# Kernel tuning notes

Hardware: AMD Instinct MI355X
Metric: run time of the kernel (lower is better)

Reference implementation:

```python
import jax, jax.numpy as jnp
import numpy as np

EPS = 1e-5
C, FR, T = 256, 7, 251  # channel, frequency, time
B = 32


def _bn(x, p, axis):
    # p: stacked [gamma, beta, running_mean, running_var] (eval-mode BatchNorm)
    g, b, m, v = p
    scale = g * jax.lax.rsqrt(v + EPS)
    shape = [1] * x.ndim
    shape[axis] = -1
    return x * scale.reshape(shape) + (b - m * scale).reshape(shape)


def _branch(xr, qw, qbn, kw, kbn, lbn):
    # xr: [N, Cin, L]. conv1x1 (no bias) + BN1d over channel axis.
    q = _bn(jnp.einsum('oc,ncl->nol', qw, xr), qbn, 1)
    k = _bn(jnp.einsum('oc,ncl->nol', kw, xr), kbn, 1)
    # adaptive_avg_pool2d((1, L)) on [N,1,Cin,L]: mean over channel axis, identity on L
    qv = q.mean(axis=1)  # [N, L]
    kv = k.mean(axis=1)  # [N, L]
    logits = qv[:, :, None] * kv[:, None, :]  # outer product == matmul(q^T, k): [N, L, L]
    g, b, m, v = lbn[:, 0]  # BatchNorm2d(1), eval mode -> scalar affine
    scale = g * jax.lax.rsqrt(v + EPS)
    w = jax.nn.softmax(logits * scale + (b - m * scale), axis=-1)
    # einsum 'bhxy,ihh->bhxy' == v * sum_i diag(w_i); return the diagonal sum [L]
    return jnp.einsum('nii->i', w)


def setup_inputs() -> dict:
    key = jax.random.key(0)
    ks = jax.random.split(key, 20)

    def w(k, o, i):
        return jax.random.normal(k, (o, i), jnp.float32) * 0.05

    def bn(k, n):
        k1, k2, k3, k4 = jax.random.split(k, 4)
        gamma = 1.0 + 0.1 * jax.random.normal(k1, (n,), jnp.float32)
        beta = 0.1 * jax.random.normal(k2, (n,), jnp.float32)
        mean = 0.1 * jax.random.normal(k3, (n,), jnp.float32)
        var = jnp.abs(1.0 + 0.1 * jax.random.normal(k4, (n,), jnp.float32))
        return jnp.stack([gamma, beta, mean, var])

    return {
        'x': jax.random.normal(ks[0], (B, C, FR, T), jnp.float32),
        'qc_w': w(ks[1], T, T), 'qc_bn': bn(ks[2], T),
        'kc_w': w(ks[3], T, T), 'kc_bn': bn(ks[4], T),
        'lc_bn': bn(ks[5], 1),
        'qf_w': w(ks[6], C, C), 'qf_bn': bn(ks[7], C),
        'kf_w': w(ks[8], C, C), 'kf_bn': bn(ks[9], C),
        'lf_bn': bn(ks[10], 1),
        'qt_w': w(ks[11], C, C), 'qt_bn': bn(ks[12], C),
        'kt_w': w(ks[13], C, C), 'kt_bn': bn(ks[14], C),
        'lt_bn': bn(ks[15], 1),
        'v_w': w(ks[16], C, C),
        'v_b': 0.05 * jax.random.normal(ks[17], (C,), jnp.float32),
        'v_bn': bn(ks[18], C),
    }


def reference(x, qc_w, qc_bn, kc_w, kc_bn, lc_bn,
              qf_w, qf_bn, kf_w, kf_bn, lf_bn,
              qt_w, qt_bn, kt_w, kt_bn, lt_bn,
              v_w, v_b, v_bn):
    b = x.shape[0]
    # x: [B, C, FR, T]
    x_c = x.transpose(0, 2, 3, 1).reshape(b * FR, T, C)   # conv over T channels
    x_f = x.transpose(0, 2, 1, 3).reshape(b * FR, C, T)   # conv over C channels
    x_t = x.transpose(0, 3, 1, 2).reshape(b * T, C, FR)   # conv over C channels
    dc = _branch(x_c, qc_w, qc_bn, kc_w, kc_bn, lc_bn)    # [C] (attention over channel axis of v)
    df = _branch(x_f, qf_w, qf_bn, kf_w, kf_bn, lf_bn)    # [T]
    dt = _branch(x_t, qt_w, qt_bn, kt_w, kt_bn, lt_bn)    # [FR]
    v = _bn(jnp.einsum('oc,bcxy->boxy', v_w, x) + v_b[None, :, None, None], v_bn, 1)
    # v_c + v_f + v_t + x, where each v_* = v scaled by summed attention diagonal
    return v * (dc[None, :, None, None] + dt[None, None, :, None] + df[None, None, None, :]) + x
```

## Files before the change

kernel.cpp:

```cpp
#include <hip/hip_runtime.h>

typedef unsigned short u16;
typedef __attribute__((ext_vector_type(8))) short short8;
typedef __attribute__((ext_vector_type(4))) float float4v;
typedef __attribute__((ext_vector_type(4))) int int4v;
typedef __attribute__((ext_vector_type(2))) int int2v;

#define EPS 1e-5f
#define NC 256
#define NT 251
#define NF 7
#define NSP 1757
#define NB 32

#define OFF_QEC 0
#define OFF_KEC 256
#define OFF_QEF 512
#define OFF_KEF 768
#define OFF_QET 1024
#define OFF_KET 1280
#define OFF_VSC 1536
#define OFF_VOF 1792
#define OFF_CONST 2048
#define OFF_DC 2064
#define OFF_DF 2320
#define OFF_DT 2576
#define WS_END 2592
#define OFF_QT 2592
#define OFF_KT (OFF_QT+56320)
#define WS2_END (OFF_KT+56320)
#define OFF_WB16 WS2_END
#define WS3_END (WS2_END+32768)

__device__ __forceinline__ u16 f2b(float f) {
    unsigned int u = __float_as_uint(f);
    return (u16)((u + 0x7FFFu + ((u >> 16) & 1u)) >> 16);
}

__global__ __launch_bounds__(256) void prep_kernel(
    const float* qc_w, const float* qc_bn, const float* kc_w, const float* kc_bn, const float* lc_bn,
    const float* qf_w, const float* qf_bn, const float* kf_w, const float* kf_bn, const float* lf_bn,
    const float* qt_w, const float* qt_bn, const float* kt_w, const float* kt_bn, const float* lt_bn,
    const float* v_b, const float* v_bn, const float* v_w, float* ws)
{
    int tid = threadIdx.x;
    int blk = blockIdx.x;
    __shared__ float sc[256];
    __shared__ float red[256];
    if (blk < 24) {
        int m = blk >> 2, j = blk & 3;
        const float* w; const float* bn; float* out; int O;
        switch (m) {
            case 0: w=qc_w; bn=qc_bn; out=ws+OFF_QEC; O=NT; break;
            case 1: w=kc_w; bn=kc_bn; out=ws+OFF_KEC; O=NT; break;
            case 2: w=qf_w; bn=qf_bn; out=ws+OFF_QEF; O=NC; break;
            case 3: w=kf_w; bn=kf_bn; out=ws+OFF_KEF; O=NC; break;
            case 4: w=qt_w; bn=qt_bn; out=ws+OFF_QET; O=NC; break;
            default: w=kt_w; bn=kt_bn; out=ws+OFF_KET; O=NC; break;
        }
        if (tid < O) sc[tid] = bn[tid] * rsqrtf(bn[3*O+tid] + EPS);
        __syncthreads();
        int tl = tid & 63, kc4 = tid >> 6;
        int t = j*64 + tl;
        float acc = 0.f;
        if (t < O) {
            #pragma unroll 8
            for (int o = kc4; o < O; o += 4)
                acc = fmaf(sc[o], w[(size_t)o*O + t], acc);
        }
        red[tid] = acc;
        __syncthreads();
        if (tid < 64) {
            int tt = j*64 + tid;
            if (tt < O)
                out[tt] = (red[tid] + red[tid+64] + red[tid+128] + red[tid+192]) / (float)O;
        }
    } else if (blk == 24) {
        if (tid < NC) {
            float s = v_bn[tid] * rsqrtf(v_bn[3*NC+tid] + EPS);
            ws[OFF_VSC+tid] = s;
            ws[OFF_VOF+tid] = v_bn[NC+tid] - v_bn[2*NC+tid]*s + v_b[tid]*s;
        }
        if (tid == 0) {
            ws[OFF_CONST+6] = lc_bn[0] * rsqrtf(lc_bn[3] + EPS);
            ws[OFF_CONST+7] = lf_bn[0] * rsqrtf(lf_bn[3] + EPS);
            ws[OFF_CONST+8] = lt_bn[0] * rsqrtf(lt_bn[3] + EPS);
        }
        for (int i = tid; i < WS_END - OFF_DC; i += 256) ws[OFF_DC + i] = 0.f;
        const float* bns[6] = {qc_bn, kc_bn, qf_bn, kf_bn, qt_bn, kt_bn};
        #pragma unroll
        for (int m2 = 0; m2 < 6; ++m2) {
            int O = (m2 < 2) ? NT : NC;
            const float* bn = bns[m2];
            float bs = 0.f;
            if (tid < O) {
                float s = bn[tid] * rsqrtf(bn[3*O+tid] + EPS);
                bs = bn[O+tid] - bn[2*O+tid]*s;
            }
            red[tid] = bs; __syncthreads();
            for (int s2 = 128; s2 > 0; s2 >>= 1) { if (tid < s2) red[tid] += red[tid+s2]; __syncthreads(); }
            if (tid == 0) ws[OFF_CONST+m2] = red[0] / (float)O;
            __syncthreads();
        }
    } else {
        u16* wb = (u16*)(ws + OFF_WB16);
        int base = (blk - 25) * 8192;
        for (int i = tid; i < 8192; i += 256) {
            int idx = base + i;
            int r = idx >> 12, q = idx & 4095;
            int o = ((r >> 3) << 7) + ((q >> 9) << 4) + ((q >> 3) & 15);
            int k = ((r & 7) << 5) + (((q >> 7) & 3) << 3) + (q & 7);
            wb[idx] = f2b(v_w[o*NC + k]);
        }
    }
}

__global__ __launch_bounds__(512) void qkt_kernel(const float* __restrict__ x,
                                                  float* __restrict__ ws, int fuse_t)
{
    __shared__ float kvc[NC];
    __shared__ float kvf[NT];
    int tid = threadIdx.x;
    int n = blockIdx.x;
    int b = n / NF, f = n % NF;
    const float* xb = x + (size_t)b*NC*NSP + (size_t)f*NT;
    const float* cst = ws + OFF_CONST;

    float qc = 0.f, kc = 0.f, qf = 0.f, kf = 0.f;

    if (tid < 256) {
        const float* xrow = xb + (size_t)tid*NSP;
        const float* qeC = ws + OFF_QEC;  const float* keC = ws + OFF_KEC;
        #pragma unroll 16
        for (int t = 0; t < NT; ++t) {
            float xv = xrow[t];
            qc = fmaf(qeC[t], xv, qc);
            kc = fmaf(keC[t], xv, kc);
        }
        qc += cst[0]; kc += cst[1];
        kvc[tid] = kc;
    } else if (tid - 256 < NT) {
        int t = tid - 256;
        const float* xc = xb + t;
        const float* qeF = ws + OFF_QEF;  const float* keF = ws + OFF_KEF;
        const float* qeT = ws + OFF_QET;  const float* keT = ws + OFF_KET;
        float qt = 0.f, kt = 0.f;
        #pragma unroll 8
        for (int ch = 0; ch < NC; ++ch) {
            float xv = xc[(size_t)ch*NSP];
            qf = fmaf(qeF[ch], xv, qf);
            kf = fmaf(keF[ch], xv, kf);
            qt = fmaf(qeT[ch], xv, qt);
            kt = fmaf(keT[ch], xv, kt);
        }
        qf += cst[2]; kf += cst[3];
        qt += cst[4]; kt += cst[5];
        kvf[t] = kf;
        if (fuse_t) {
            ws[OFF_QT + ((size_t)b*NT + t)*NF + f] = qt;
            ws[OFF_KT + ((size_t)b*NT + t)*NF + f] = kt;
        }
    }
    __syncthreads();

    if (tid < 256) {
        float s = cst[6];
        float qi = s * qc;
        float m0=-1e30f, m1=-1e30f, m2=-1e30f, m3=-1e30f;
        #pragma unroll 2
        for (int jj = 0; jj < NC; jj += 4) {
            m0 = fmaxf(m0, qi*kvc[jj]);
            m1 = fmaxf(m1, qi*kvc[jj+1]);
            m2 = fmaxf(m2, qi*kvc[jj+2]);
            m3 = fmaxf(m3, qi*kvc[jj+3]);
        }
        float m = fmaxf(fmaxf(m0,m1), fmaxf(m2,m3));
        float d0=0.f, d1=0.f, d2=0.f, d3=0.f;
        #pragma unroll 2
        for (int jj = 0; jj < NC; jj += 4) {
            d0 += __expf(qi*kvc[jj]   - m);
            d1 += __expf(qi*kvc[jj+1] - m);
            d2 += __expf(qi*kvc[jj+2] - m);
            d3 += __expf(qi*kvc[jj+3] - m);
        }
        float den = (d0+d1)+(d2+d3);
        atomicAdd(&ws[OFF_DC + tid], __expf(qi*kc - m)/den);
    } else if (tid - 256 < NT) {
        int t = tid - 256;
        float s = cst[7];
        float qi = s * qf;
        float m0=-1e30f, m1=-1e30f, m2=-1e30f, m3=-1e30f;
        int jj = 0;
        #pragma unroll 2
        for (; jj + 3 < NT; jj += 4) {
            m0 = fmaxf(m0, qi*kvf[jj]);
            m1 = fmaxf(m1, qi*kvf[jj+1]);
            m2 = fmaxf(m2, qi*kvf[jj+2]);
            m3 = fmaxf(m3, qi*kvf[jj+3]);
        }
        for (; jj < NT; ++jj) m0 = fmaxf(m0, qi*kvf[jj]);
        float m = fmaxf(fmaxf(m0,m1), fmaxf(m2,m3));
        float d0=0.f, d1=0.f, d2=0.f, d3=0.f;
        jj = 0;
        #pragma unroll 2
        for (; jj + 3 < NT; jj += 4) {
            d0 += __expf(qi*kvf[jj]   - m);
            d1 += __expf(qi*kvf[jj+1] - m);
            d2 += __expf(qi*kvf[jj+2] - m);
            d3 += __expf(qi*kvf[jj+3] - m);
        }
        for (; jj < NT; ++jj) d0 += __expf(qi*kvf[jj] - m);
        float den = (d0+d1)+(d2+d3);
        atomicAdd(&ws[OFF_DF + t], __expf(qi*kf - m)/den);
    }
}

__global__ __launch_bounds__(256) void tsm_kernel(float* __restrict__ ws)
{
    __shared__ float dt_acc[NF];
    int tid = threadIdx.x, b = blockIdx.x;
    if (tid < NF) dt_acc[tid] = 0.f;
    __syncthreads();
    if (tid < NT) {
        float s = ws[OFF_CONST+8];
        const float* qp = ws + OFF_QT + ((size_t)b*NT + tid)*NF;
        const float* kp = ws + OFF_KT + ((size_t)b*NT + tid)*NF;
        float q[NF], k[NF];
        #pragma unroll
        for (int i = 0; i < NF; ++i) { q[i] = qp[i]; k[i] = kp[i]; }
        #pragma unroll
        for (int i = 0; i < NF; ++i) {
            float qi = s * q[i];
            float m = -1e30f;
            #pragma unroll
            for (int j = 0; j < NF; ++j) m = fmaxf(m, qi*k[j]);
            float den = 0.f;
            #pragma unroll
            for (int j = 0; j < NF; ++j) den += __expf(qi*k[j] - m);
            atomicAdd(&dt_acc[i], __expf(qi*k[i] - m)/den);
        }
    }
    __syncthreads();
    if (tid < NF) atomicAdd(&ws[OFF_DT + tid], dt_acc[tid]);
}

__global__ __launch_bounds__(256) void t_kernel(const float* __restrict__ x, float* __restrict__ ws)
{
    __shared__ float qs[32*NF], ks[32*NF], dt_acc[NF];
    int tid = threadIdx.x;
    int b  = blockIdx.x >> 3;
    int t0 = (blockIdx.x & 7) * 32;
    int tl = tid & 31, fr = tid >> 5;
    int t = t0 + tl;
    bool act = (fr < NF) && (t < NT);
    if (tid < NF) dt_acc[tid] = 0.f;

    float aq = 0.f, ak = 0.f;
    const float* qeT = ws + OFF_QET;
    const float* keT = ws + OFF_KET;
    if (act) {
        const float* xr = x + (size_t)b*NC*NSP + fr*NT + t;
        #pragma unroll 8
        for (int ch = 0; ch < NC; ++ch) {
            float xv = xr[(size_t)ch*NSP];
            aq = fmaf(qeT[ch], xv, aq);
            ak = fmaf(keT[ch], xv, ak);
        }
    }
    __syncthreads();
    if (act) {
        qs[tl*NF + fr] = aq + ws[OFF_CONST+4];
        ks[tl*NF + fr] = ak + ws[OFF_CONST+5];
    }
    __syncthreads();
    if (act) {
        float s = ws[OFF_CONST+8];
        float qi = s * qs[tl*NF + fr];
        float m = -1e30f;
        #pragma unroll
        for (int j = 0; j < NF; ++j) m = fmaxf(m, qi*ks[tl*NF + j]);
        float den = 0.f;
        #pragma unroll
        for (int j = 0; j < NF; ++j) den += __expf(qi*ks[tl*NF + j] - m);
        atomicAdd(&dt_acc[fr], __expf(qi*ks[tl*NF + fr] - m)/den);
    }
    __syncthreads();
    if (tid < NF) atomicAdd(&ws[OFF_DT + tid], dt_acc[tid]);
}

template<int WBF>
__global__ __launch_bounds__(256) void main_kernel(
    const float* __restrict__ x, const float* __restrict__ vw,
    const float* __restrict__ ws, float* __restrict__ out)
{
    __shared__ u16 Ws[8*512];
    __shared__ unsigned int Xs[8*256];
    __shared__ float vsL[128], voL[128], dcL[128], dtfL[128];

    int tid = threadIdx.x;
    int n0 = blockIdx.x * 128;
    int o0 = blockIdx.y * 128;
    int b  = blockIdx.z;
    const size_t xbase = (size_t)b * NC * NSP;

    if (tid < 128) {
        int o = o0 + tid;
        vsL[tid] = ws[OFF_VSC+o];
        voL[tid] = ws[OFF_VOF+o];
        dcL[tid] = ws[OFF_DC+o];
        int nn = n0 + tid; if (nn > NSP-1) nn = NSP-1;
        int ff = nn / NT, tt = nn - ff*NT;
        dtfL[tid] = ws[OFF_DT+ff] + ws[OFF_DF+tt];
    }

    int wv = tid >> 6, ln = tid & 63;
    int quad = ln >> 4, l16 = ln & 15;
    int wr = wv >> 1, wc = wv & 1;

    float4v acc[4][4] = {};

    int kgs = tid >> 5, nbs = tid & 31;
    int oo = tid >> 1, half = tid & 1;

    const u16* wbg = nullptr;
    if constexpr (WBF) wbg = (const u16*)(ws + OFF_WB16) + (size_t)blockIdx.y * 32768;

    for (int ks = 0; ks < 8; ++ks) {
        int k0 = ks * 32;
        if constexpr (WBF) {
            const int4v* wsrc = (const int4v*)(wbg + (size_t)ks*4096);
            *(int4v*)&Ws[tid*8]        = wsrc[tid];
            *(int4v*)&Ws[2048 + tid*8] = wsrc[256 + tid];
        } else {
            const float* wr4 = vw + (size_t)(o0+oo)*NC + k0 + half*16;
            union { u16 us[16]; short8 v[2]; } wb;
            #pragma unroll
            for (int c = 0; c < 16; ++c) wb.us[c] = f2b(wr4[c]);
            int frg = oo >> 4, o16 = oo & 15;
            #pragma unroll
            for (int qq = 0; qq < 2; ++qq) {
                int qd = 2*half + qq;
                *(short8*)&Ws[frg*512 + qd*128 + o16*8] = wb.v[qq];
            }
        }
        {
            int nbase = n0 + nbs*4;
            const float* xr = x + xbase + (size_t)(k0 + kgs*4)*NSP + nbase;
            float xv[4][4];
            if (nbase + 3 < NSP) {
                #pragma unroll
                for (int rr = 0; rr < 4; ++rr)
                    #pragma unroll
                    for (int i = 0; i < 4; ++i)
                        xv[rr][i] = xr[(size_t)rr*NSP + i];
            } else {
                #pragma unroll
                for (int rr = 0; rr < 4; ++rr)
                    #pragma unroll
                    for (int i = 0; i < 4; ++i)
                        xv[rr][i] = (nbase + i < NSP) ? xr[(size_t)rr*NSP + i] : 0.f;
            }
            unsigned int pk[8];
            #pragma unroll
            for (int i = 0; i < 4; ++i)
                #pragma unroll
                for (int jp = 0; jp < 2; ++jp)
                    pk[i*2+jp] = (unsigned int)f2b(xv[2*jp][i])
                               | ((unsigned int)f2b(xv[2*jp+1][i]) << 16);
            *(int4v*)&Xs[kgs*256 + nbs*8]     = *(int4v*)&pk[0];
            *(int4v*)&Xs[kgs*256 + nbs*8 + 4] = *(int4v*)&pk[4];
        }
        __syncthreads();

        short8 afr[4], bfr[4];
        #pragma unroll
        for (int fr = 0; fr < 4; ++fr)
            afr[fr] = *(short8*)&Ws[(wr*4+fr)*512 + ln*8];
        #pragma unroll
        for (int fc = 0; fc < 4; ++fc) {
            int nn = wc*64 + fc*16 + l16;
            int2v lo = *(int2v*)&Xs[(2*quad)*256 + nn*2];
            int2v hi = *(int2v*)&Xs[(2*quad+1)*256 + nn*2];
            union { int i4[4]; short8 v; } u;
            u.i4[0] = lo.x; u.i4[1] = lo.y; u.i4[2] = hi.x; u.i4[3] = hi.y;
            bfr[fc] = u.v;
        }
        #pragma unroll
        for (int fr = 0; fr < 4; ++fr)
            #pragma unroll
            for (int fc = 0; fc < 4; ++fc)
                acc[fr][fc] = __builtin_amdgcn_mfma_f32_16x16x32_bf16(
                    afr[fr], bfr[fc], acc[fr][fc], 0, 0, 0);
        __syncthreads();
    }

    #pragma unroll
    for (int fr = 0; fr < 4; ++fr) {
        #pragma unroll
        for (int r = 0; r < 4; ++r) {
            int ol = wr*64 + fr*16 + quad*4 + r;
            int o = o0 + ol;
            float vs = vsL[ol], vo = voL[ol], dcv = dcL[ol];
            const size_t orow = xbase + (size_t)o*NSP;
            #pragma unroll
            for (int fc = 0; fc < 4; ++fc) {
                int nl = wc*64 + fc*16 + l16;
                int nn = n0 + nl;
                if (nn < NSP) {
                    size_t gi = orow + nn;
                    out[gi] = (acc[fr][fc][r]*vs + vo)*(dcv + dtfL[nl]) + x[gi];
                }
            }
        }
    }
}

extern "C" void kernel_launch(void* const* d_in, const int* in_sizes, int n_in,
                              void* d_out, int out_size, void* d_ws, size_t ws_size,
                              hipStream_t stream)
{
    const float* x    = (const float*)d_in[0];
    const float* qc_w = (const float*)d_in[1];  const float* qc_bn = (const float*)d_in[2];
    const float* kc_w = (const float*)d_in[3];  const float* kc_bn = (const float*)d_in[4];
    const float* lc_bn= (const float*)d_in[5];
    const float* qf_w = (const float*)d_in[6];  const float* qf_bn = (const float*)d_in[7];
    const float* kf_w = (const float*)d_in[8];  const float* kf_bn = (const float*)d_in[9];
    const float* lf_bn= (const float*)d_in[10];
    const float* qt_w = (const float*)d_in[11]; const float* qt_bn = (const float*)d_in[12];
    const float* kt_w = (const float*)d_in[13]; const float* kt_bn = (const float*)d_in[14];
    const float* lt_bn= (const float*)d_in[15];
    const float* v_w  = (const float*)d_in[16]; const float* v_b   = (const float*)d_in[17];
    const float* v_bn = (const float*)d_in[18];
    float* ws = (float*)d_ws;
    float* out = (float*)d_out;

    int fuse_t = (ws_size >= (size_t)WS2_END * sizeof(float)) ? 1 : 0;
    int wbf    = (ws_size >= (size_t)WS3_END * sizeof(float)) ? 1 : 0;

    prep_kernel<<<wbf ? 33 : 25, 256, 0, stream>>>(qc_w,qc_bn,kc_w,kc_bn,lc_bn,
                                                   qf_w,qf_bn,kf_w,kf_bn,lf_bn,
                                                   qt_w,qt_bn,kt_w,kt_bn,lt_bn,
                                                   v_b,v_bn,v_w,ws);
    qkt_kernel<<<NB*NF, 512, 0, stream>>>(x, ws, fuse_t);
    if (fuse_t) tsm_kernel<<<NB, 256, 0, stream>>>(ws);
    else        t_kernel<<<NB*8, 256, 0, stream>>>(x, ws);
    if (wbf) main_kernel<1><<<dim3(14, 2, NB), 256, 0, stream>>>(x, v_w, ws, out);
    else     main_kernel<0><<<dim3(14, 2, NB), 256, 0, stream>>>(x, v_w, ws, out);
}
```

Baseline: 253.4 us.

## Double-buffer GEMM tiles, swizzle LDS, split qkt blocks, remap grid per XCD

The main GEMM kernel now double-buffers its weight and x tiles in LDS, issuing global loads for the next k-step before running the MFMAs on the current one. It also XOR-swizzles the Xs layout to cut bank conflicts and remaps the 1D grid so both o-halves of a tile land on the same XCD for L2 reuse. The qkt kernel is split into two blocks per (b,f), one per branch, each dividing its reduction across 512 threads, and the BN bias-mean reductions move from one serial block into the per-matrix prep blocks. The costs are more LDS, higher register pressure from holding prefetched data, and a remapping that assumes an 8-XCD round-robin dispatch.

```diff
diff --git a/kernel.cpp b/kernel.cpp
--- a/kernel.cpp
+++ b/kernel.cpp
@@ -32,6 +32,8 @@
 #define OFF_WB16 WS2_END
 #define WS3_END (WS2_END+32768)
 
+#define XSW(kg, w) ((kg)*256 + ((w) ^ ((((kg)>>1)&3)<<3)))
+
 __device__ __forceinline__ u16 f2b(float f) {
     unsigned int u = __float_as_uint(f);
     return (u16)((u + 0x7FFFu + ((u >> 16) & 1u)) >> 16);
@@ -75,6 +77,14 @@
             if (tt < O)
                 out[tt] = (red[tid] + red[tid+64] + red[tid+128] + red[tid+192]) / (float)O;
         }
+        if (j == 0) {
+            float bs = 0.f;
+            if (tid < O) bs = bn[O+tid] - bn[2*O+tid]*sc[tid];
+            __syncthreads();
+            red[tid] = bs; __syncthreads();
+            for (int s2 = 128; s2 > 0; s2 >>= 1) { if (tid < s2) red[tid] += red[tid+s2]; __syncthreads(); }
+            if (tid == 0) ws[OFF_CONST+m] = red[0] / (float)O;
+        }
     } else if (blk == 24) {
         if (tid < NC) {
             float s = v_bn[tid] * rsqrtf(v_bn[3*NC+tid] + EPS);
@@ -87,21 +97,6 @@
             ws[OFF_CONST+8] = lt_bn[0] * rsqrtf(lt_bn[3] + EPS);
         }
         for (int i = tid; i < WS_END - OFF_DC; i += 256) ws[OFF_DC + i] = 0.f;
-        const float* bns[6] = {qc_bn, kc_bn, qf_bn, kf_bn, qt_bn, kt_bn};
-        #pragma unroll
-        for (int m2 = 0; m2 < 6; ++m2) {
-            int O = (m2 < 2) ? NT : NC;
-            const float* bn = bns[m2];
-            float bs = 0.f;
-            if (tid < O) {
-                float s = bn[tid] * rsqrtf(bn[3*O+tid] + EPS);
-                bs = bn[O+tid] - bn[2*O+tid]*s;
-            }
-            red[tid] = bs; __syncthreads();
-            for (int s2 = 128; s2 > 0; s2 >>= 1) { if (tid < s2) red[tid] += red[tid+s2]; __syncthreads(); }
-            if (tid == 0) ws[OFF_CONST+m2] = red[0] / (float)O;
-            __syncthreads();
-        }
     } else {
         u16* wb = (u16*)(ws + OFF_WB16);
         int base = (blk - 25) * 8192;
@@ -118,100 +113,115 @@
 __global__ __launch_bounds__(512) void qkt_kernel(const float* __restrict__ x,
                                                   float* __restrict__ ws, int fuse_t)
 {
-    __shared__ float kvc[NC];
-    __shared__ float kvf[NT];
+    __shared__ float kv[NC];
+    __shared__ float p0[512], p1[512], p2[512], p3[512];
     int tid = threadIdx.x;
-    int n = blockIdx.x;
+    int bid = blockIdx.x;
+    int n = bid >> 1, role = bid & 1;
     int b = n / NF, f = n % NF;
     const float* xb = x + (size_t)b*NC*NSP + (size_t)f*NT;
     const float* cst = ws + OFF_CONST;
-
-    float qc = 0.f, kc = 0.f, qf = 0.f, kf = 0.f;
-
-    if (tid < 256) {
-        const float* xrow = xb + (size_t)tid*NSP;
+    int half = tid >> 8, lid = tid & 255;
+
+    if (role == 0) {
+        const float* xrow = xb + (size_t)lid*NSP;
         const float* qeC = ws + OFF_QEC;  const float* keC = ws + OFF_KEC;
+        float qc = 0.f, kc = 0.f;
+        int t0 = half ? 126 : 0, t1 = half ? NT : 126;
         #pragma unroll 16
-        for (int t = 0; t < NT; ++t) {
+        for (int t = t0; t < t1; ++t) {
             float xv = xrow[t];
             qc = fmaf(qeC[t], xv, qc);
             kc = fmaf(keC[t], xv, kc);
         }
-        qc += cst[0]; kc += cst[1];
-        kvc[tid] = kc;
-    } else if (tid - 256 < NT) {
-        int t = tid - 256;
-        const float* xc = xb + t;
-        const float* qeF = ws + OFF_QEF;  const float* keF = ws + OFF_KEF;
-        const float* qeT = ws + OFF_QET;  const float* keT = ws + OFF_KET;
-        float qt = 0.f, kt = 0.f;
-        #pragma unroll 8
-        for (int ch = 0; ch < NC; ++ch) {
-            float xv = xc[(size_t)ch*NSP];
-            qf = fmaf(qeF[ch], xv, qf);
-            kf = fmaf(keF[ch], xv, kf);
-            qt = fmaf(qeT[ch], xv, qt);
-            kt = fmaf(keT[ch], xv, kt);
-        }
-        qf += cst[2]; kf += cst[3];
-        qt += cst[4]; kt += cst[5];
-        kvf[t] = kf;
-        if (fuse_t) {
-            ws[OFF_QT + ((size_t)b*NT + t)*NF + f] = qt;
-            ws[OFF_KT + ((size_t)b*NT + t)*NF + f] = kt;
-        }
-    }
-    __syncthreads();
-
-    if (tid < 256) {
-        float s = cst[6];
-        float qi = s * qc;
-        float m0=-1e30f, m1=-1e30f, m2=-1e30f, m3=-1e30f;
-        #pragma unroll 2
-        for (int jj = 0; jj < NC; jj += 4) {
-            m0 = fmaxf(m0, qi*kvc[jj]);
-            m1 = fmaxf(m1, qi*kvc[jj+1]);
-            m2 = fmaxf(m2, qi*kvc[jj+2]);
-            m3 = fmaxf(m3, qi*kvc[jj+3]);
-        }
-        float m = fmaxf(fmaxf(m0,m1), fmaxf(m2,m3));
-        float d0=0.f, d1=0.f, d2=0.f, d3=0.f;
-        #pragma unroll 2
-        for (int jj = 0; jj < NC; jj += 4) {
-            d0 += __expf(qi*kvc[jj]   - m);
-            d1 += __expf(qi*kvc[jj+1] - m);
-            d2 += __expf(qi*kvc[jj+2] - m);
-            d3 += __expf(qi*kvc[jj+3] - m);
-        }
-        float den = (d0+d1)+(d2+d3);
-        atomicAdd(&ws[OFF_DC + tid], __expf(qi*kc - m)/den);
-    } else if (tid - 256 < NT) {
-        int t = tid - 256;
-        float s = cst[7];
-        float qi = s * qf;
-        float m0=-1e30f, m1=-1e30f, m2=-1e30f, m3=-1e30f;
-        int jj = 0;
-        #pragma unroll 2
-        for (; jj + 3 < NT; jj += 4) {
-            m0 = fmaxf(m0, qi*kvf[jj]);
-            m1 = fmaxf(m1, qi*kvf[jj+1]);
-            m2 = fmaxf(m2, qi*kvf[jj+2]);
-            m3 = fmaxf(m3, qi*kvf[jj+3]);
-        }
-        for (; jj < NT; ++jj) m0 = fmaxf(m0, qi*kvf[jj]);
-        float m = fmaxf(fmaxf(m0,m1), fmaxf(m2,m3));
-        float d0=0.f, d1=0.f, d2=0.f, d3=0.f;
-        jj = 0;
-        #pragma unroll 2
-        for (; jj + 3 < NT; jj += 4) {
-            d0 += __expf(qi*kvf[jj]   - m);
-            d1 += __expf(qi*kvf[jj+1] - m);
-            d2 += __expf(qi*kvf[jj+2] - m);
-            d3 += __expf(qi*kvf[jj+3] - m);
-        }
-        for (; jj < NT; ++jj) d0 += __expf(qi*kvf[jj] - m);
-        float den = (d0+d1)+(d2+d3);
-        atomicAdd(&ws[OFF_DF + t], __expf(qi*kf - m)/den);
+        p0[tid] = qc; p1[tid] = kc;
+        __syncthreads();
+        if (tid < 256) {
+            qc = p0[tid] + p0[tid+256] + cst[0];
+            kc = p1[tid] + p1[tid+256] + cst[1];
+            kv[tid] = kc;
+        }
+        __syncthreads();
+        if (tid < 256) {
+            float s = cst[6];
+            float qi = s * qc;
+            float m0=-1e30f, m1=-1e30f, m2=-1e30f, m3=-1e30f;
+            #pragma unroll 2
+            for (int jj = 0; jj < NC; jj += 4) {
+                m0 = fmaxf(m0, qi*kv[jj]);
+                m1 = fmaxf(m1, qi*kv[jj+1]);
+                m2 = fmaxf(m2, qi*kv[jj+2]);
+                m3 = fmaxf(m3, qi*kv[jj+3]);
+            }
+            float m = fmaxf(fmaxf(m0,m1), fmaxf(m2,m3));
+            float d0=0.f, d1=0.f, d2=0.f, d3=0.f;
+            #pragma unroll 2
+            for (int jj = 0; jj < NC; jj += 4) {
+                d0 += __expf(qi*kv[jj]   - m);
+                d1 += __expf(qi*kv[jj+1] - m);
+                d2 += __expf(qi*kv[jj+2] - m);
+                d3 += __expf(qi*kv[jj+3] - m);
+            }
+            float den = (d0+d1)+(d2+d3);
+            atomicAdd(&ws[OFF_DC + tid], __expf(qi*kv[tid] - m)/den);
+        }
+    } else {
+        float qf=0.f, kf=0.f, qt=0.f, kt=0.f;
+        if (lid < NT) {
+            const float* xc = xb + lid + (size_t)(half*128)*NSP;
+            const float* qeF = ws + OFF_QEF + half*128;  const float* keF = ws + OFF_KEF + half*128;
+            const float* qeT = ws + OFF_QET + half*128;  const float* keT = ws + OFF_KET + half*128;
+            #pragma unroll 8
+            for (int ch = 0; ch < 128; ++ch) {
+                float xv = xc[(size_t)ch*NSP];
+                qf = fmaf(qeF[ch], xv, qf);
+                kf = fmaf(keF[ch], xv, kf);
+                qt = fmaf(qeT[ch], xv, qt);
+                kt = fmaf(keT[ch], xv, kt);
+            }
+        }
+        p0[tid]=qf; p1[tid]=kf; p2[tid]=qt; p3[tid]=kt;
+        __syncthreads();
+        float qfv=0.f, kfv=0.f;
+        if (tid < NT) {
+            qfv = p0[tid] + p0[tid+256] + cst[2];
+            kfv = p1[tid] + p1[tid+256] + cst[3];
+            float qtv = p2[tid] + p2[tid+256] + cst[4];
+            float ktv = p3[tid] + p3[tid+256] + cst[5];
+            kv[tid] = kfv;
+            if (fuse_t) {
+                ws[OFF_QT + ((size_t)b*NT + tid)*NF + f] = qtv;
+                ws[OFF_KT + ((size_t)b*NT + tid)*NF + f] = ktv;
+            }
+        }
+        __syncthreads();
+        if (tid < NT) {
+            float s = cst[7];
+            float qi = s * qfv;
+            float m0=-1e30f, m1=-1e30f, m2=-1e30f, m3=-1e30f;
+            int jj = 0;
+            #pragma unroll 2
+            for (; jj + 3 < NT; jj += 4) {
+                m0 = fmaxf(m0, qi*kv[jj]);
+                m1 = fmaxf(m1, qi*kv[jj+1]);
+                m2 = fmaxf(m2, qi*kv[jj+2]);
+                m3 = fmaxf(m3, qi*kv[jj+3]);
+            }
+            for (; jj < NT; ++jj) m0 = fmaxf(m0, qi*kv[jj]);
+            float m = fmaxf(fmaxf(m0,m1), fmaxf(m2,m3));
+            float d0=0.f, d1=0.f, d2=0.f, d3=0.f;
+            jj = 0;
+            #pragma unroll 2
+            for (; jj + 3 < NT; jj += 4) {
+                d0 += __expf(qi*kv[jj]   - m);
+                d1 += __expf(qi*kv[jj+1] - m);
+                d2 += __expf(qi*kv[jj+2] - m);
+                d3 += __expf(qi*kv[jj+3] - m);
+            }
+            for (; jj < NT; ++jj) d0 += __expf(qi*kv[jj] - m);
+            float den = (d0+d1)+(d2+d3);
+            atomicAdd(&ws[OFF_DF + tid], __expf(qi*kfv - m)/den);
+        }
     }
 }
 
@@ -293,14 +303,17 @@
     const float* __restrict__ x, const float* __restrict__ vw,
     const float* __restrict__ ws, float* __restrict__ out)
 {
-    __shared__ u16 Ws[8*512];
-    __shared__ unsigned int Xs[8*256];
+    __shared__ u16 Ws[2][4096];
+    __shared__ unsigned int Xs[2][2048];
     __shared__ float vsL[128], voL[128], dcL[128], dtfL[128];
 
     int tid = threadIdx.x;
-    int n0 = blockIdx.x * 128;
-    int o0 = blockIdx.y * 128;
-    int b  = blockIdx.z;
+    int flat = blockIdx.x;
+    int xcd = flat & 7, idx = flat >> 3;
+    int pair = xcd*56 + (idx >> 1);
+    int o0 = (idx & 1) * 128;
+    int n0 = (pair % 14) * 128;
+    int b  = pair / 14;
     const size_t xbase = (size_t)b * NC * NSP;
 
     if (tid < 128) {
@@ -323,64 +336,82 @@
     int oo = tid >> 1, half = tid & 1;
 
     const u16* wbg = nullptr;
-    if constexpr (WBF) wbg = (const u16*)(ws + OFF_WB16) + (size_t)blockIdx.y * 32768;
-
-    for (int ks = 0; ks < 8; ++ks) {
-        int k0 = ks * 32;
+    if constexpr (WBF) wbg = (const u16*)(ws + OFF_WB16) + (size_t)(o0 >> 7) * 32768;
+
+    int4v wA, wB;
+    float wf[16];
+    float xv[4][4];
+
+    auto loadW = [&](int ks) {
         if constexpr (WBF) {
             const int4v* wsrc = (const int4v*)(wbg + (size_t)ks*4096);
-            *(int4v*)&Ws[tid*8]        = wsrc[tid];
-            *(int4v*)&Ws[2048 + tid*8] = wsrc[256 + tid];
+            wA = wsrc[tid]; wB = wsrc[256 + tid];
         } else {
-            const float* wr4 = vw + (size_t)(o0+oo)*NC + k0 + half*16;
+            const float* wr4 = vw + (size_t)(o0+oo)*NC + ks*32 + half*16;
+            #pragma unroll
+            for (int c = 0; c < 16; ++c) wf[c] = wr4[c];
+        }
+    };
+    auto loadX = [&](int ks) {
+        int nbase = n0 + nbs*4;
+        const float* xr = x + xbase + (size_t)(ks*32 + kgs*4)*NSP + nbase;
+        if (nbase + 3 < NSP) {
+            #pragma unroll
+            for (int rr = 0; rr < 4; ++rr)
+                #pragma unroll
+                for (int i = 0; i < 4; ++i)
+                    xv[rr][i] = xr[(size_t)rr*NSP + i];
+        } else {
+            #pragma unroll
+            for (int rr = 0; rr < 4; ++rr)
+                #pragma unroll
+                for (int i = 0; i < 4; ++i)
+                    xv[rr][i] = (nbase + i < NSP) ? xr[(size_t)rr*NSP + i] : 0.f;
+        }
+    };
+    auto storeWX = [&](int bufi) {
+        if constexpr (WBF) {
+            *(int4v*)&Ws[bufi][tid*8]        = wA;
+            *(int4v*)&Ws[bufi][2048 + tid*8] = wB;
+        } else {
             union { u16 us[16]; short8 v[2]; } wb;
             #pragma unroll
-            for (int c = 0; c < 16; ++c) wb.us[c] = f2b(wr4[c]);
+            for (int c = 0; c < 16; ++c) wb.us[c] = f2b(wf[c]);
             int frg = oo >> 4, o16 = oo & 15;
             #pragma unroll
             for (int qq = 0; qq < 2; ++qq) {
                 int qd = 2*half + qq;
-                *(short8*)&Ws[frg*512 + qd*128 + o16*8] = wb.v[qq];
-            }
-        }
-        {
-            int nbase = n0 + nbs*4;
-            const float* xr = x + xbase + (size_t)(k0 + kgs*4)*NSP + nbase;
-            float xv[4][4];
-            if (nbase + 3 < NSP) {
-                #pragma unroll
-                for (int rr = 0; rr < 4; ++rr)
-                    #pragma unroll
-                    for (int i = 0; i < 4; ++i)
-                        xv[rr][i] = xr[(size_t)rr*NSP + i];
-            } else {
-                #pragma unroll
-                for (int rr = 0; rr < 4; ++rr)
-                    #pragma unroll
-                    for (int i = 0; i < 4; ++i)
-                        xv[rr][i] = (nbase + i < NSP) ? xr[(size_t)rr*NSP + i] : 0.f;
-            }
-            unsigned int pk[8];
-            #pragma unroll
-            for (int i = 0; i < 4; ++i)
-                #pragma unroll
-                for (int jp = 0; jp < 2; ++jp)
-                    pk[i*2+jp] = (unsigned int)f2b(xv[2*jp][i])
-                               | ((unsigned int)f2b(xv[2*jp+1][i]) << 16);
-            *(int4v*)&Xs[kgs*256 + nbs*8]     = *(int4v*)&pk[0];
-            *(int4v*)&Xs[kgs*256 + nbs*8 + 4] = *(int4v*)&pk[4];
-        }
-        __syncthreads();
+                *(short8*)&Ws[bufi][frg*512 + qd*128 + o16*8] = wb.v[qq];
+            }
+        }
+        unsigned int pk[8];
+        #pragma unroll
+        for (int i = 0; i < 4; ++i)
+            #pragma unroll
+            for (int jp = 0; jp < 2; ++jp)
+                pk[i*2+jp] = (unsigned int)f2b(xv[2*jp][i])
+                           | ((unsigned int)f2b(xv[2*jp+1][i]) << 16);
+        *(int4v*)&Xs[bufi][XSW(kgs, nbs*8)]     = *(int4v*)&pk[0];
+        *(int4v*)&Xs[bufi][XSW(kgs, nbs*8 + 4)] = *(int4v*)&pk[4];
+    };
+
+    loadW(0); loadX(0);
+    storeWX(0);
+    __syncthreads();
+
+    for (int ks = 0; ks < 8; ++ks) {
+        int cur = ks & 1;
+        if (ks < 7) { loadW(ks+1); loadX(ks+1); }
 
         short8 afr[4], bfr[4];
         #pragma unroll
         for (int fr = 0; fr < 4; ++fr)
-            afr[fr] = *(short8*)&Ws[(wr*4+fr)*512 + ln*8];
+            afr[fr] = *(short8*)&Ws[cur][(wr*4+fr)*512 + ln*8];
         #pragma unroll
         for (int fc = 0; fc < 4; ++fc) {
             int nn = wc*64 + fc*16 + l16;
-            int2v lo = *(int2v*)&Xs[(2*quad)*256 + nn*2];
-            int2v hi = *(int2v*)&Xs[(2*quad+1)*256 + nn*2];
+            int2v lo = *(int2v*)&Xs[cur][XSW(2*quad,   2*nn)];
+            int2v hi = *(int2v*)&Xs[cur][XSW(2*quad+1, 2*nn)];
             union { int i4[4]; short8 v; } u;
             u.i4[0] = lo.x; u.i4[1] = lo.y; u.i4[2] = hi.x; u.i4[3] = hi.y;
             bfr[fc] = u.v;
@@ -391,6 +422,8 @@
             for (int fc = 0; fc < 4; ++fc)
                 acc[fr][fc] = __builtin_amdgcn_mfma_f32_16x16x32_bf16(
                     afr[fr], bfr[fc], acc[fr][fc], 0, 0, 0);
+
+        if (ks < 7) storeWX(cur ^ 1);
         __syncthreads();
     }
 
@@ -441,9 +474,9 @@
                                                    qf_w,qf_bn,kf_w,kf_bn,lf_bn,
                                                    qt_w,qt_bn,kt_w,kt_bn,lt_bn,
                                                    v_b,v_bn,v_w,ws);
-    qkt_kernel<<<NB*NF, 512, 0, stream>>>(x, ws, fuse_t);
+    qkt_kernel<<<NB*NF*2, 512, 0, stream>>>(x, ws, fuse_t);
     if (fuse_t) tsm_kernel<<<NB, 256, 0, stream>>>(ws);
     else        t_kernel<<<NB*8, 256, 0, stream>>>(x, ws);
-    if (wbf) main_kernel<1><<<dim3(14, 2, NB), 256, 0, stream>>>(x, v_w, ws, out);
-    else     main_kernel<0><<<dim3(14, 2, NB), 256, 0, stream>>>(x, v_w, ws, out);
-}
+    if (wbf) main_kernel<1><<<896, 256, 0, stream>>>(x, v_w, ws, out);
+    else     main_kernel<0><<<896, 256, 0, stream>>>(x, v_w, ws, out);
+}
```

New measurement: 245.5 us. 3.1% less time.
